# Performance work log

Hardware: AMD Instinct MI355X
Metric: run time of the kernel (lower is better)

## Reference

```python
import jax, jax.numpy as jnp
import numpy as np

N_NODES = 100000
N_EMBED = 256
N_HIDDEN = 256
N_EDGES = 1600000


def setup_inputs() -> dict:
    key = jax.random.key(0)
    k_emb, k_w1, k_w2, k_ei = jax.random.split(key, 4)
    # Learned parameters. PyG ChebConv(K=1) holds one bias-free Linear per
    # Chebyshev order plus a shared bias; at K=1 that is a single W and b.
    emb = jax.random.normal(k_emb, (N_NODES, N_EMBED), dtype=jnp.float32)
    W1 = jax.random.normal(k_w1, (N_EMBED, N_HIDDEN), dtype=jnp.float32) * 0.05
    b1 = jnp.zeros((N_HIDDEN,), dtype=jnp.float32)
    W2 = jax.random.normal(k_w2, (N_HIDDEN, N_HIDDEN), dtype=jnp.float32) * 0.05
    b2 = jnp.zeros((N_HIDDEN,), dtype=jnp.float32)
    prop_edge_index = jax.random.randint(k_ei, (2, N_EDGES), 0, N_NODES, dtype=jnp.int64)
    return {"emb": emb, "W1": W1, "b1": b1, "W2": W2, "b2": b2,
            "prop_edge_index": prop_edge_index}


def reference(emb, W1, b1, W2, b2, prop_edge_index):
    # ChebConv with K=1: only Tx_0 = x is used, so each conv is x @ W + b.
    # edge_index affects only the (unused) Laplacian normalization at K=1.
    # Dropout is identity (training=False for a deterministic reference).
    x = jax.nn.relu(emb @ W1 + b1)          # [N, H] conv1 + ReLU
    out = x @ W2 + b2                        # [N, H] conv2
    return out
```

## Files before the change

kernel.cpp:

```cpp
#include <hip/hip_runtime.h>

#define M_NODES 100000

typedef float  f32x4  __attribute__((ext_vector_type(4)));
typedef short  bf16x8 __attribute__((ext_vector_type(8)));
typedef unsigned short u16x4 __attribute__((ext_vector_type(4)));

__device__ __forceinline__ unsigned short f2bf(float f) {
  union { float f; unsigned int u; } v; v.f = f;
  unsigned int u = v.u;
  return (unsigned short)((u + 0x7FFFu + ((u >> 16) & 1u)) >> 16);
}

__global__ void prep_w_kernel(const float* __restrict__ W1, const float* __restrict__ W2,
                              unsigned short* __restrict__ R1, unsigned short* __restrict__ R2) {
  int b = blockIdx.x;
  const float* W = (b < 64) ? W1 : W2;
  unsigned short* R = (b < 64) ? R1 : R2;
  int e  = ((b & 63) * 256 + (int)threadIdx.x) * 4;
  int n  = e >> 8;
  int k0 = e & 255;
  u16x4 h;
  #pragma unroll
  for (int i = 0; i < 4; ++i) h[i] = f2bf(W[(k0 + i) * 256 + n]);
  int kt = k0 >> 6, kl = k0 & 63;
  int off = kt * 16384 + n * 64 + (((kl >> 3) ^ (n & 7)) << 3) + (kl & 7);
  *(u16x4*)(R + off) = h;
}

template <int PASS>
__global__ __launch_bounds__(256, 2)
void cheb_gemm(const float* __restrict__ Af32,
               const unsigned short* __restrict__ Aimg,
               const unsigned short* __restrict__ Wimg,
               const float* __restrict__ bias,
               unsigned short* __restrict__ Hout,
               float* __restrict__ Cout)
{
  __shared__ unsigned short lds[40960];
  unsigned short* Ab0 = lds;
  unsigned short* Ab1 = lds + 4096;
  unsigned short* Wb0 = lds + 8192;
  unsigned short* Wb1 = lds + 24576;

  const int tid  = threadIdx.x;
  const int lane = tid & 63;
  const int w    = tid >> 6;
  const int rb   = blockIdx.x;

  f32x4 acc[4][4] = {};
  f32x4 areg[4];

  auto stageW = [&](int kt, unsigned short* dst) {
    const unsigned short* src = Wimg + kt * 16384;
    #pragma unroll
    for (int it = 0; it < 8; ++it) {
      int chunk = it * 4 + w;
      __builtin_amdgcn_global_load_lds(
          (const __attribute__((address_space(1))) unsigned int*)(const void*)(src + chunk * 512 + lane * 8),
          (__attribute__((address_space(3))) unsigned int*)(void*)(dst + chunk * 512),
          16, 0, 0);
    }
  };
  auto stageA2 = [&](int kt, unsigned short* dst) {
    const unsigned short* src = Aimg + (size_t)(rb * 4 + kt) * 4096;
    #pragma unroll
    for (int it = 0; it < 2; ++it) {
      int chunk = it * 4 + w;
      __builtin_amdgcn_global_load_lds(
          (const __attribute__((address_space(1))) unsigned int*)(const void*)(src + chunk * 512 + lane * 8),
          (__attribute__((address_space(3))) unsigned int*)(void*)(dst + chunk * 512),
          16, 0, 0);
    }
  };
  auto loadA1 = [&](int kt) {
    #pragma unroll
    for (int i = 0; i < 4; ++i) {
      int e = (i * 256 + tid) * 4;
      int r = e >> 6, c = e & 63;
      int grow = rb * 64 + r;
      f32x4 v = {0.f, 0.f, 0.f, 0.f};
      if (grow < M_NODES) v = *(const f32x4*)(Af32 + (size_t)grow * 256 + kt * 64 + c);
      areg[i] = v;
    }
  };
  auto writeA1 = [&](unsigned short* dst) {
    #pragma unroll
    for (int i = 0; i < 4; ++i) {
      int e = (i * 256 + tid) * 4;
      int r = e >> 6, c = e & 63;
      u16x4 h;
      #pragma unroll
      for (int j = 0; j < 4; ++j) h[j] = f2bf(areg[i][j]);
      int off = r * 64 + (((c >> 3) ^ (r & 7)) << 3) + (c & 7);
      *(u16x4*)(dst + off) = h;
    }
  };
  auto compute = [&](const unsigned short* A, const unsigned short* B) {
    #pragma unroll
    for (int kk = 0; kk < 2; ++kk) {
      bf16x8 a[4], b[4];
      #pragma unroll
      for (int mi = 0; mi < 4; ++mi) {
        int r = mi * 16 + (lane & 15);
        int slot = (kk * 4 + (lane >> 4)) ^ (r & 7);
        a[mi] = *(const bf16x8*)(A + r * 64 + slot * 8);
      }
      #pragma unroll
      for (int ni = 0; ni < 4; ++ni) {
        int n = w * 64 + ni * 16 + (lane & 15);
        int slot = (kk * 4 + (lane >> 4)) ^ (n & 7);
        b[ni] = *(const bf16x8*)(B + n * 64 + slot * 8);
      }
      #pragma unroll
      for (int mi = 0; mi < 4; ++mi)
        #pragma unroll
        for (int ni = 0; ni < 4; ++ni)
          acc[mi][ni] = __builtin_amdgcn_mfma_f32_16x16x32_bf16(a[mi], b[ni], acc[mi][ni], 0, 0, 0);
    }
  };

  if (PASS == 1) { loadA1(0); writeA1(Ab0); } else { stageA2(0, Ab0); }
  stageW(0, Wb0);
  __syncthreads();

  #pragma unroll
  for (int kt = 0; kt < 4; ++kt) {
    unsigned short* Acur = (kt & 1) ? Ab1 : Ab0;
    unsigned short* Anxt = (kt & 1) ? Ab0 : Ab1;
    unsigned short* Wcur = (kt & 1) ? Wb1 : Wb0;
    unsigned short* Wnxt = (kt & 1) ? Wb0 : Wb1;
    if (kt < 3) {
      if (PASS == 1) loadA1(kt + 1); else stageA2(kt + 1, Anxt);
      stageW(kt + 1, Wnxt);
    }
    compute(Acur, Wcur);
    if (PASS == 1 && kt < 3) writeA1(Anxt);
    __syncthreads();
  }

  float bn[4];
  #pragma unroll
  for (int ni = 0; ni < 4; ++ni) bn[ni] = bias[w * 64 + ni * 16 + (lane & 15)];

  if (PASS == 1) {
    unsigned short* img = Hout + (size_t)(rb * 4 + w) * 4096;
    #pragma unroll
    for (int mi = 0; mi < 4; ++mi)
      #pragma unroll
      for (int ni = 0; ni < 4; ++ni)
        #pragma unroll
        for (int rg = 0; rg < 4; ++rg) {
          int r = mi * 16 + (lane >> 4) * 4 + rg;
          int k = ni * 16 + (lane & 15);
          float v = acc[mi][ni][rg] + bn[ni];
          v = fmaxf(v, 0.f);
          int off = r * 64 + (((k >> 3) ^ (r & 7)) << 3) + (k & 7);
          img[off] = f2bf(v);
        }
  } else {
    #pragma unroll
    for (int mi = 0; mi < 4; ++mi)
      #pragma unroll
      for (int rg = 0; rg < 4; ++rg) {
        int r = mi * 16 + (lane >> 4) * 4 + rg;
        int grow = rb * 64 + r;
        if (grow < M_NODES) {
          #pragma unroll
          for (int ni = 0; ni < 4; ++ni) {
            int col = w * 64 + ni * 16 + (lane & 15);
            Cout[(size_t)grow * 256 + col] = acc[mi][ni][rg] + bn[ni];
          }
        }
      }
  }
}

extern "C" void kernel_launch(void* const* d_in, const int* in_sizes, int n_in,
                              void* d_out, int out_size, void* d_ws, size_t ws_size,
                              hipStream_t stream) {
  const float* emb = (const float*)d_in[0];
  const float* W1  = (const float*)d_in[1];
  const float* b1  = (const float*)d_in[2];
  const float* W2  = (const float*)d_in[3];
  const float* b2  = (const float*)d_in[4];
  float* out = (float*)d_out;

  unsigned short* Wr1  = (unsigned short*)d_ws;
  unsigned short* Wr2  = Wr1 + 65536;
  unsigned short* Himg = Wr2 + 65536;

  prep_w_kernel<<<128, 256, 0, stream>>>(W1, W2, Wr1, Wr2);

  const int grid = (M_NODES + 63) / 64;
  cheb_gemm<1><<<grid, 256, 0, stream>>>(emb, nullptr, Wr1, b1, Himg, nullptr);
  cheb_gemm<2><<<grid, 256, 0, stream>>>(nullptr, Himg, Wr2, b2, nullptr, out);
}
```

Before: 81.23 us.

## Fuse both GEMM layers into one kernel keeping hidden activations in LDS

Replaces the two-pass GEMM, which wrote the bf16 hidden activations to global memory and read them back, with one fused kernel. Each 512-thread block handles 128 rows and writes relu(XW1+b1) into a 64KB LDS buffer that aliases the A staging buffers. It then runs the second GEMM from LDS while streaming W2 tiles. This removes the intermediate global round-trip and one kernel launch, at the cost of 128KB of LDS per block, which limits occupancy, and an extra barrier between the two phases.

```diff
diff --git a/kernel.cpp b/kernel.cpp
--- a/kernel.cpp
+++ b/kernel.cpp
@@ -1,6 +1,8 @@
 #include <hip/hip_runtime.h>
 
 #define M_NODES 100000
+#define BM 128
+#define NBLK ((M_NODES + BM - 1) / BM)
 
 typedef float  f32x4  __attribute__((ext_vector_type(4)));
 typedef short  bf16x8 __attribute__((ext_vector_type(8)));
@@ -28,66 +30,57 @@
   *(u16x4*)(R + off) = h;
 }
 
-template <int PASS>
-__global__ __launch_bounds__(256, 2)
-void cheb_gemm(const float* __restrict__ Af32,
-               const unsigned short* __restrict__ Aimg,
-               const unsigned short* __restrict__ Wimg,
-               const float* __restrict__ bias,
-               unsigned short* __restrict__ Hout,
-               float* __restrict__ Cout)
+__global__ __launch_bounds__(512, 2)
+void cheb_fused(const float* __restrict__ X,
+                const unsigned short* __restrict__ W1img,
+                const unsigned short* __restrict__ W2img,
+                const float* __restrict__ b1,
+                const float* __restrict__ b2,
+                float* __restrict__ out)
 {
-  __shared__ unsigned short lds[40960];
-  unsigned short* Ab0 = lds;
-  unsigned short* Ab1 = lds + 4096;
-  unsigned short* Wb0 = lds + 8192;
-  unsigned short* Wb1 = lds + 24576;
+  __shared__ unsigned short lds[65536];
+  unsigned short* Hbuf = lds;
+  unsigned short* Ab0  = lds;
+  unsigned short* Ab1  = lds + 8192;
+  unsigned short* Wb0  = lds + 32768;
+  unsigned short* Wb1  = lds + 49152;
 
   const int tid  = threadIdx.x;
   const int lane = tid & 63;
   const int w    = tid >> 6;
+  const int wr   = w >> 2;
+  const int wc   = w & 3;
   const int rb   = blockIdx.x;
 
   f32x4 acc[4][4] = {};
   f32x4 areg[4];
 
-  auto stageW = [&](int kt, unsigned short* dst) {
-    const unsigned short* src = Wimg + kt * 16384;
-    #pragma unroll
-    for (int it = 0; it < 8; ++it) {
-      int chunk = it * 4 + w;
+  auto stageW = [&](const unsigned short* img, int kt, unsigned short* dst) {
+    const unsigned short* src = img + kt * 16384;
+    #pragma unroll
+    for (int it = 0; it < 4; ++it) {
+      int chunk = it * 8 + w;
       __builtin_amdgcn_global_load_lds(
           (const __attribute__((address_space(1))) unsigned int*)(const void*)(src + chunk * 512 + lane * 8),
           (__attribute__((address_space(3))) unsigned int*)(void*)(dst + chunk * 512),
           16, 0, 0);
     }
   };
-  auto stageA2 = [&](int kt, unsigned short* dst) {
-    const unsigned short* src = Aimg + (size_t)(rb * 4 + kt) * 4096;
-    #pragma unroll
-    for (int it = 0; it < 2; ++it) {
-      int chunk = it * 4 + w;
-      __builtin_amdgcn_global_load_lds(
-          (const __attribute__((address_space(1))) unsigned int*)(const void*)(src + chunk * 512 + lane * 8),
-          (__attribute__((address_space(3))) unsigned int*)(void*)(dst + chunk * 512),
-          16, 0, 0);
-    }
-  };
-  auto loadA1 = [&](int kt) {
+  auto loadA = [&](int kt) {
     #pragma unroll
     for (int i = 0; i < 4; ++i) {
-      int e = (i * 256 + tid) * 4;
+      int e = (i * 512 + tid) * 4;
       int r = e >> 6, c = e & 63;
-      int grow = rb * 64 + r;
+      int grow = rb * BM + r;
       f32x4 v = {0.f, 0.f, 0.f, 0.f};
-      if (grow < M_NODES) v = *(const f32x4*)(Af32 + (size_t)grow * 256 + kt * 64 + c);
+      if (grow < M_NODES) v = *(const f32x4*)(X + (size_t)grow * 256 + kt * 64 + c);
       areg[i] = v;
     }
   };
-  auto writeA1 = [&](unsigned short* dst) {
+  auto writeA = [&](unsigned short* dst) {
     #pragma unroll
     for (int i = 0; i < 4; ++i) {
-      int e = (i * 256 + tid) * 4;
+      int e = (i * 512 + tid) * 4;
       int r = e >> 6, c = e & 63;
       u16x4 h;
       #pragma unroll
@@ -96,19 +89,20 @@
       *(u16x4*)(dst + off) = h;
     }
   };
-  auto compute = [&](const unsigned short* A, const unsigned short* B) {
+  auto compute = [&](const unsigned short* Abase, int rstride, int slotbase,
+                     const unsigned short* B) {
     #pragma unroll
     for (int kk = 0; kk < 2; ++kk) {
       bf16x8 a[4], b[4];
       #pragma unroll
       for (int mi = 0; mi < 4; ++mi) {
-        int r = mi * 16 + (lane & 15);
-        int slot = (kk * 4 + (lane >> 4)) ^ (r & 7);
-        a[mi] = *(const bf16x8*)(A + r * 64 + slot * 8);
+        int r = wr * 64 + mi * 16 + (lane & 15);
+        int slot = (slotbase + kk * 4 + (lane >> 4)) ^ (r & 7);
+        a[mi] = *(const bf16x8*)(Abase + r * rstride + slot * 8);
       }
       #pragma unroll
       for (int ni = 0; ni < 4; ++ni) {
-        int n = w * 64 + ni * 16 + (lane & 15);
+        int n = wc * 64 + ni * 16 + (lane & 15);
         int slot = (kk * 4 + (lane >> 4)) ^ (n & 7);
         b[ni] = *(const bf16x8*)(B + n * 64 + slot * 8);
       }
@@ -120,8 +114,9 @@
     }
   };
 
-  if (PASS == 1) { loadA1(0); writeA1(Ab0); } else { stageA2(0, Ab0); }
-  stageW(0, Wb0);
+  loadA(0);
+  stageW(W1img, 0, Wb0);
+  writeA(Ab0);
   __syncthreads();
 
   #pragma unroll
@@ -131,45 +126,61 @@
     unsigned short* Wcur = (kt & 1) ? Wb1 : Wb0;
     unsigned short* Wnxt = (kt & 1) ? Wb0 : Wb1;
     if (kt < 3) {
-      if (PASS == 1) loadA1(kt + 1); else stageA2(kt + 1, Anxt);
-      stageW(kt + 1, Wnxt);
-    }
-    compute(Acur, Wcur);
-    if (PASS == 1 && kt < 3) writeA1(Anxt);
+      loadA(kt + 1);
+      stageW(W1img, kt + 1, Wnxt);
+    } else {
+      stageW(W2img, 0, Wnxt);
+    }
+    compute(Acur, 64, 0, Wcur);
+    if (kt < 3) writeA(Anxt);
     __syncthreads();
   }
 
-  float bn[4];
-  #pragma unroll
-  for (int ni = 0; ni < 4; ++ni) bn[ni] = bias[w * 64 + ni * 16 + (lane & 15)];
-
-  if (PASS == 1) {
-    unsigned short* img = Hout + (size_t)(rb * 4 + w) * 4096;
+  {
+    float bn[4];
+    #pragma unroll
+    for (int ni = 0; ni < 4; ++ni) bn[ni] = b1[wc * 64 + ni * 16 + (lane & 15)];
     #pragma unroll
     for (int mi = 0; mi < 4; ++mi)
       #pragma unroll
-      for (int ni = 0; ni < 4; ++ni)
+      for (int ni = 0; ni < 4; ++ni) {
+        int k = wc * 64 + ni * 16 + (lane & 15);
         #pragma unroll
         for (int rg = 0; rg < 4; ++rg) {
-          int r = mi * 16 + (lane >> 4) * 4 + rg;
-          int k = ni * 16 + (lane & 15);
-          float v = acc[mi][ni][rg] + bn[ni];
-          v = fmaxf(v, 0.f);
-          int off = r * 64 + (((k >> 3) ^ (r & 7)) << 3) + (k & 7);
-          img[off] = f2bf(v);
+          int r = wr * 64 + mi * 16 + (lane >> 4) * 4 + rg;
+          float v = fmaxf(acc[mi][ni][rg] + bn[ni], 0.f);
+          int off = r * 256 + (((k >> 3) ^ (r & 7)) << 3) + (k & 7);
+          Hbuf[off] = f2bf(v);
+          acc[mi][ni][rg] = 0.f;
         }
-  } else {
+      }
+  }
+  __syncthreads();
+
+  #pragma unroll
+  for (int kt = 0; kt < 4; ++kt) {
+    unsigned short* Wcur = (kt & 1) ? Wb1 : Wb0;
+    unsigned short* Wnxt = (kt & 1) ? Wb0 : Wb1;
+    if (kt < 3) stageW(W2img, kt + 1, Wnxt);
+    compute(Hbuf, 256, kt * 8, Wcur);
+    if (kt < 3) __syncthreads();
+  }
+
+  {
+    float bn[4];
+    #pragma unroll
+    for (int ni = 0; ni < 4; ++ni) bn[ni] = b2[wc * 64 + ni * 16 + (lane & 15)];
     #pragma unroll
     for (int mi = 0; mi < 4; ++mi)
       #pragma unroll
       for (int rg = 0; rg < 4; ++rg) {
-        int r = mi * 16 + (lane >> 4) * 4 + rg;
-        int grow = rb * 64 + r;
+        int r = wr * 64 + mi * 16 + (lane >> 4) * 4 + rg;
+        int grow = rb * BM + r;
         if (grow < M_NODES) {
           #pragma unroll
           for (int ni = 0; ni < 4; ++ni) {
-            int col = w * 64 + ni * 16 + (lane & 15);
-            Cout[(size_t)grow * 256 + col] = acc[mi][ni][rg] + bn[ni];
+            int col = wc * 64 + ni * 16 + (lane & 15);
+            out[(size_t)grow * 256 + col] = acc[mi][ni][rg] + bn[ni];
           }
         }
       }
@@ -186,13 +197,9 @@
   const float* b2  = (const float*)d_in[4];
   float* out = (float*)d_out;
 
-  unsigned short* Wr1  = (unsigned short*)d_ws;
-  unsigned short* Wr2  = Wr1 + 65536;
-  unsigned short* Himg = Wr2 + 65536;
+  unsigned short* Wr1 = (unsigned short*)d_ws;
+  unsigned short* Wr2 = Wr1 + 65536;
 
   prep_w_kernel<<<128, 256, 0, stream>>>(W1, W2, Wr1, Wr2);
-
-  const int grid = (M_NODES + 63) / 64;
-  cheb_gemm<1><<<grid, 256, 0, stream>>>(emb, nullptr, Wr1, b1, Himg, nullptr);
-  cheb_gemm<2><<<grid, 256, 0, stream>>>(nullptr, Himg, Wr2, b2, nullptr, out);
-}
+  cheb_fused<<<NBLK, 512, 0, stream>>>(emb, Wr1, Wr2, b1, b2, out);
+}
```

Measured after the change: 74.86 us. -7.8%, faster.
